# Optimization experiments

Measured on AMD Instinct MI355X. Metric: run time of the kernel, lower is better.

## Reference

```python
import jax, jax.numpy as jnp
import numpy as np

B, C, P = 16, 512, 4096


def setup_inputs() -> dict:
    key = jax.random.key(0)
    ks = jax.random.split(key, 7)
    s = 1.0 / np.sqrt(C)  # torch Conv1d default init scale
    return {
        "x": jax.random.normal(ks[0], (B, C, P), dtype=jnp.float32),
        "Wq": jax.random.uniform(ks[1], (C, C), jnp.float32, -s, s),
        "bq": jax.random.uniform(ks[2], (C,), jnp.float32, -s, s),
        "Wk": jax.random.uniform(ks[3], (C, C), jnp.float32, -s, s),
        "bk": jax.random.uniform(ks[4], (C,), jnp.float32, -s, s),
        "Wv": jax.random.uniform(ks[5], (C, C), jnp.float32, -s, s),
        "bv": jax.random.uniform(ks[6], (C,), jnp.float32, -s, s),
    }


def reference(x, Wq, bq, Wk, bk, Wv, bv):
    # 1x1 Conv1d == channel-mixing GEMM: out[b,o,p] = sum_i W[o,i] x[b,i,p] + b[o]
    q = jnp.einsum('oi,bip->bop', Wq, x) + bq[None, :, None]   # [B,C,P]
    k = jnp.einsum('oi,bip->bop', Wk, x) + bk[None, :, None]   # [B,C,P]
    v = jnp.einsum('oi,bip->bop', Wv, x) + bv[None, :, None]   # [B,C,P]
    energy = jnp.einsum('bcp,bdp->bcd', q, k)                  # [B,C,C] (unscaled)
    attn = jax.nn.softmax(energy, axis=-1)
    out = jnp.einsum('bcd,bdp->bcp', attn, v)                  # [B,C,P]
    return out
```

## Files before the change

kernel.cpp:

```cpp
#include <hip/hip_runtime.h>
#include <hip/hip_bf16.h>

#define CD 512
#define PD 4096
#define BD 16
#define GKS 8
#define NTRI 10

typedef __bf16 bf16x8 __attribute__((ext_vector_type(8)));
typedef float f32x4 __attribute__((ext_vector_type(4)));
typedef unsigned short u16x8 __attribute__((ext_vector_type(8)));
typedef unsigned short u16x4 __attribute__((ext_vector_type(4)));

__device__ __forceinline__ unsigned short f2bf(float f) {
  unsigned u = __builtin_bit_cast(unsigned, f);
  u += 0x7FFFu + ((u >> 16) & 1u);
  return (unsigned short)(u >> 16);
}
__device__ __forceinline__ float bf2f(unsigned short h) {
  unsigned u = ((unsigned)h) << 16;
  return __builtin_bit_cast(float, u);
}

__global__ void convert_w2(const float* __restrict__ Wq, const float* __restrict__ Wk,
                           unsigned short* __restrict__ Wqh, unsigned short* __restrict__ Wql,
                           unsigned short* __restrict__ Wkh, unsigned short* __restrict__ Wkl) {
  int i = blockIdx.x * 256 + threadIdx.x;
  if (i >= CD * CD) return;
  float q = Wq[i]; unsigned short qh = f2bf(q);
  Wqh[i] = qh; Wql[i] = f2bf(q - bf2f(qh));
  float k = Wk[i]; unsigned short kh = f2bf(k);
  Wkh[i] = kh; Wkl[i] = f2bf(k - bf2f(kh));
}

__global__ void transpose_wv(const float* __restrict__ Wv, unsigned short* __restrict__ Wvt) {
  __shared__ float tile[64][65];
  int o0 = blockIdx.x * 64, j0 = blockIdx.y * 64;
  int t = threadIdx.x, r = t >> 2, g = t & 3;
  const float* src = Wv + (size_t)(o0 + r) * CD + j0 + g * 16;
#pragma unroll
  for (int i = 0; i < 16; ++i) tile[r][g * 16 + i] = src[i];
  __syncthreads();
  u16x8 th[2];
#pragma unroll
  for (int i = 0; i < 16; ++i) th[i >> 3][i & 7] = f2bf(tile[g * 16 + i][r]);
  unsigned short* dst = Wvt + (size_t)(j0 + r) * CD + o0 + g * 16;
  *reinterpret_cast<u16x8*>(dst) = th[0];
  *reinterpret_cast<u16x8*>(dst + 8) = th[1];
}

__global__ void convert_x_stream(const float* __restrict__ x, unsigned short* __restrict__ xsh,
                                 unsigned short* __restrict__ xsl, float* __restrict__ r_part) {
  int z = blockIdx.y, c = blockIdx.x;
  int t = threadIdx.x;
  size_t rowo = ((size_t)z * CD + c) * PD;
  const float* src = x + rowo + t * 16;
  f32x4 v4[4];
  float s = 0.f;
#pragma unroll
  for (int j = 0; j < 4; ++j) {
    v4[j] = *reinterpret_cast<const f32x4*>(src + j * 4);
    s += v4[j][0] + v4[j][1] + v4[j][2] + v4[j][3];
  }
  u16x8 h[2], l[2];
#pragma unroll
  for (int j = 0; j < 4; ++j)
#pragma unroll
    for (int i = 0; i < 4; ++i) {
      int e = j * 4 + i;
      float f = v4[j][i];
      unsigned short hh = f2bf(f);
      h[e >> 3][e & 7] = hh;
      l[e >> 3][e & 7] = f2bf(f - bf2f(hh));
    }
  unsigned short* ph = xsh + rowo + t * 16;
  unsigned short* pl = xsl + rowo + t * 16;
  *reinterpret_cast<u16x8*>(ph) = h[0];
  *reinterpret_cast<u16x8*>(ph + 8) = h[1];
  *reinterpret_cast<u16x8*>(pl) = l[0];
  *reinterpret_cast<u16x8*>(pl + 8) = l[1];
  s += __shfl_xor(s, 1);
  s += __shfl_xor(s, 2);
  if ((t & 3) == 0) r_part[((size_t)z * CD + c) * 64 + (t >> 2)] = s;
}

__global__ void transpose_xh(const unsigned short* __restrict__ xsh,
                             unsigned short* __restrict__ xth) {
  __shared__ unsigned short sh[64][72];
  int z = blockIdx.z;
  int p0 = blockIdx.x * 64, c0 = blockIdx.y * 64;
  int t = threadIdx.x, r = t >> 2, g = t & 3;
  const unsigned short* src = xsh + ((size_t)z * CD + c0 + r) * PD + p0 + g * 16;
  *reinterpret_cast<u16x8*>(&sh[r][g * 16]) = *reinterpret_cast<const u16x8*>(src);
  *reinterpret_cast<u16x8*>(&sh[r][g * 16 + 8]) = *reinterpret_cast<const u16x8*>(src + 8);
  __syncthreads();
  u16x8 th[2];
#pragma unroll
  for (int i = 0; i < 16; ++i) th[i >> 3][i & 7] = sh[g * 16 + i][r];
  unsigned short* dst = xth + ((size_t)z * PD + p0 + r) * CD + c0 + g * 16;
  *reinterpret_cast<u16x8*>(dst) = th[0];
  *reinterpret_cast<u16x8*>(dst + 8) = th[1];
}

__global__ void uvw_kernel(const float* __restrict__ r_part, const float* __restrict__ Wq,
                           const float* __restrict__ bq, const float* __restrict__ Wk,
                           float* __restrict__ uw) {
  __shared__ float rl[CD];
  int z = blockIdx.x, rg = blockIdx.y;
  int t = threadIdx.x;
  for (int c = t; c < CD; c += 256) {
    const float* rp = r_part + ((size_t)z * CD + c) * 64;
    f32x4 s4 = *reinterpret_cast<const f32x4*>(rp);
#pragma unroll
    for (int pb = 4; pb < 64; pb += 4) s4 += *reinterpret_cast<const f32x4*>(rp + pb);
    rl[c] = s4[0] + s4[1] + s4[2] + s4[3];
  }
  __syncthreads();
  int lane = t & 63, w = t >> 6;
#pragma unroll
  for (int rr = 0; rr < 16; ++rr) {
    int c = rg * 64 + w * 16 + rr;
    const float* wq = Wq + (size_t)c * CD;
    const float* wk = Wk + (size_t)c * CD;
    float du = 0.f, dw = 0.f;
#pragma unroll
    for (int j = 0; j < 8; ++j) {
      float rv = rl[lane + 64 * j];
      du += wq[lane + 64 * j] * rv;
      dw += wk[lane + 64 * j] * rv;
    }
#pragma unroll
    for (int o = 32; o > 0; o >>= 1) {
      du += __shfl_xor(du, o);
      dw += __shfl_xor(dw, o);
    }
    if (lane == 0) {
      uw[(size_t)z * 2 * CD + c] = du + (float)PD * bq[c];
      uw[(size_t)z * 2 * CD + CD + c] = dw;
    }
  }
}

enum { EPI_F32 = 0, EPI_HILO = 1, EPI_BF16 = 2, EPI_ROWB = 3 };

template <int BM, int BN, int WM, int WN, int MODE, int EPI, bool TRI, int SPLITK = 1>
__global__ __launch_bounds__((BM / WM) * (BN / WN) * 64) void gemm2(
    const unsigned short* __restrict__ Ahi, const unsigned short* __restrict__ Alo,
    const unsigned short* __restrict__ Bhi, const unsigned short* __restrict__ Blo,
    long long sA, long long sB, int ldA, int ldB, int K,
    float* __restrict__ Cf, unsigned short* __restrict__ Chi, unsigned short* __restrict__ Clo,
    long long sC, int ldC, const float* __restrict__ bias, int gx, int gy) {
  constexpr int BK = 64;
  constexpr int WAVES = (BM / WM) * (BN / WN);
  constexpr int NSL = (MODE == 1) ? 2 : 1;
  constexpr int NPASS = (MODE == 2) ? 3 : 1;
  constexpr int MI = WM / 16, NI = WN / 16;
  constexpr int NWN = BN / WN;
  constexpr int CA = BM / 8, CB = BN / 8;
  constexpr int TOT = NSL * (CA + CB);
  constexpr bool COMPACT = TRI && (SPLITK > 1);
  __shared__ unsigned short lds[NSL * (BM + BN) * BK];

  int nwg = gridDim.x;
  int b = blockIdx.x;
  int q = nwg >> 3, r = nwg & 7, xcd = b & 7, pos = b >> 3;
  int wg = (xcd < r ? xcd * (q + 1) : r * (q + 1) + (xcd - r) * q) + pos;
  int bx, by, z, zc, tpi = 0, kbase = 0;
  if constexpr (TRI) {
    int tri = gy * (gy + 1) / 2;
    int perz = tri * SPLITK;
    z = wg / perz;
    int rem = wg - z * perz;
    int ks = rem / tri;
    tpi = rem - ks * tri;
    int tp = tpi;
    bx = 0;
    while (tp >= gy - bx) { tp -= gy - bx; ++bx; }
    by = bx + tp;
    kbase = ks * K;
    zc = z * SPLITK + ks;
  } else {
    by = wg % gy;
    int t2 = wg / gy;
    bx = t2 % gx;
    z = t2 / gx;
    zc = z;
  }

  const unsigned short* pA0 = Ahi + (size_t)z * sA + (size_t)bx * BM * ldA;
  const unsigned short* pB0 = Bhi + (size_t)z * sB + (size_t)by * BN * ldB;
  const unsigned short* pA1 = (MODE != 0) ? Alo + (size_t)z * sA + (size_t)bx * BM * ldA : pA0;
  const unsigned short* pB1 = (MODE != 0) ? Blo + (size_t)z * sB + (size_t)by * BN * ldB : pB0;

  int tid = threadIdx.x;
  int lane = tid & 63, wid = tid >> 6;
  int wr = wid / NWN, wc = wid % NWN;
  int lr = lane & 15, kh2 = lane >> 4;

  f32x4 acc[MI][NI] = {};

  for (int pass = 0; pass < NPASS; ++pass) {
    const unsigned short* cA = (MODE == 2 && pass == 2) ? pA1 : pA0;
    const unsigned short* cB = (MODE == 2 && pass == 1) ? pB1 : pB0;

    for (int k0 = kbase; k0 < kbase + K; k0 += BK) {
#pragma unroll
      for (int i = 0; i < TOT / WAVES; ++i) {
        int c = wid + i * WAVES;
        const unsigned short* srcb; int ldX, lofs, rb2;
        if constexpr (MODE == 1) {
          if (c < CA)            { srcb = pA0; ldX = ldA; lofs = c * 512;                  rb2 = c * 8; }
          else if (c < 2 * CA)   { srcb = pA1; ldX = ldA; lofs = BM * BK + (c - CA) * 512; rb2 = (c - CA) * 8; }
          else if (c < 2 * CA + CB) { int cc = c - 2 * CA; srcb = pB0; ldX = ldB;
                                      lofs = 2 * BM * BK + cc * 512;                       rb2 = cc * 8; }
          else                   { int cc = c - 2 * CA - CB; srcb = pB1; ldX = ldB;
                                   lofs = 2 * BM * BK + BN * BK + cc * 512;                rb2 = cc * 8; }
        } else {
          if (c < CA)            { srcb = cA; ldX = ldA; lofs = c * 512;                   rb2 = c * 8; }
          else                   { int cc = c - CA; srcb = cB; ldX = ldB;
                                   lofs = BM * BK + cc * 512;                              rb2 = cc * 8; }
        }
        int row = rb2 + (lane >> 3);
        const unsigned short* src =
            srcb + (size_t)row * ldX + k0 + (((lane & 7) ^ (row & 7)) << 3);
        __builtin_amdgcn_global_load_lds(
            (const __attribute__((address_space(1))) void*)src,
            (__attribute__((address_space(3))) void*)(lds + lofs), 16, 0, 0);
      }
      __syncthreads();

#pragma unroll
      for (int kk = 0; kk < BK / 32; ++kk) {
        bf16x8 ah[MI], al[MI], bh[NI], bl[NI];
#pragma unroll
        for (int m = 0; m < MI; ++m) {
          int row = wr * WM + m * 16 + lr;
          int so = ((((kk << 2) | kh2) ^ (row & 7)) << 3);
          ah[m] = *reinterpret_cast<const bf16x8*>(&lds[row * BK + so]);
          if constexpr (MODE == 1)
            al[m] = *reinterpret_cast<const bf16x8*>(&lds[BM * BK + row * BK + so]);
        }
#pragma unroll
        for (int n = 0; n < NI; ++n) {
          int row = wc * WN + n * 16 + lr;
          int so = ((((kk << 2) | kh2) ^ (row & 7)) << 3);
          bh[n] = *reinterpret_cast<const bf16x8*>(&lds[NSL * BM * BK + row * BK + so]);
          if constexpr (MODE == 1)
            bl[n] = *reinterpret_cast<const bf16x8*>(&lds[NSL * BM * BK + BN * BK + row * BK + so]);
        }
#pragma unroll
        for (int m = 0; m < MI; ++m)
#pragma unroll
          for (int n = 0; n < NI; ++n) {
            acc[m][n] = __builtin_amdgcn_mfma_f32_16x16x32_bf16(ah[m], bh[n], acc[m][n], 0, 0, 0);
            if constexpr (MODE == 1) {
              acc[m][n] = __builtin_amdgcn_mfma_f32_16x16x32_bf16(ah[m], bl[n], acc[m][n], 0, 0, 0);
              acc[m][n] = __builtin_amdgcn_mfma_f32_16x16x32_bf16(al[m], bh[n], acc[m][n], 0, 0, 0);
            }
          }
      }
      __syncthreads();
    }
  }

  int lg = lane >> 4;
#pragma unroll
  for (int m = 0; m < MI; ++m)
#pragma unroll
    for (int n = 0; n < NI; ++n) {
      int lcol = wc * WN + n * 16 + lr;
#pragma unroll
      for (int r4 = 0; r4 < 4; ++r4) {
        int lrow = wr * WM + m * 16 + lg * 4 + r4;
        float v = acc[m][n][r4];
        if constexpr (COMPACT) {
          size_t idx = (size_t)zc * sC + (size_t)tpi * (BM * BN) + (size_t)lrow * BN + lcol;
          Cf[idx] = v;
        } else {
          size_t idx = (size_t)zc * sC + (size_t)(bx * BM + lrow) * ldC + (by * BN + lcol);
          if constexpr (EPI == EPI_F32) {
            Cf[idx] = v;
          } else if constexpr (EPI == EPI_ROWB) {
            Cf[idx] = v + bias[(size_t)zc * CD + bx * BM + lrow];
          } else if constexpr (EPI == EPI_HILO) {
            unsigned short h = f2bf(v);
            Chi[idx] = h;
            Clo[idx] = f2bf(v - bf2f(h));
          } else {
            Chi[idx] = f2bf(v);
          }
        }
      }
    }
}

template <int KS>
__global__ void gram_reduce(const float* __restrict__ Gp,
                            unsigned short* __restrict__ Ghi, unsigned short* __restrict__ Glo) {
  int z = blockIdx.y;
  int tp = blockIdx.x;
  int b2 = tp, bx = 0;
  while (b2 >= 4 - bx) { b2 -= 4 - bx; ++bx; }
  int by = bx + b2;
  int t = threadIdx.x;
  const float* base = Gp + ((size_t)z * KS * NTRI + tp) * (128 * 128);
  size_t gb = (size_t)z * CD * CD;
#pragma unroll
  for (int it = 0; it < 16; ++it) {
    int lrow = it * 8 + (t >> 5);
    int lc = (t & 31) * 4;
    f32x4 s = *reinterpret_cast<const f32x4*>(base + (size_t)lrow * 128 + lc);
#pragma unroll
    for (int ks = 1; ks < KS; ++ks)
      s += *reinterpret_cast<const f32x4*>(base + (size_t)ks * NTRI * 128 * 128 +
                                           (size_t)lrow * 128 + lc);
    u16x4 h, l;
#pragma unroll
    for (int i = 0; i < 4; ++i) {
      unsigned short hh = f2bf(s[i]);
      h[i] = hh; l[i] = f2bf(s[i] - bf2f(hh));
    }
    size_t o = gb + (size_t)(bx * 128 + lrow) * CD + by * 128 + lc;
    *reinterpret_cast<u16x4*>(Ghi + o) = h;
    *reinterpret_cast<u16x4*>(Glo + o) = l;
  }
}

__global__ void mirror_g(unsigned short* __restrict__ Ghi, unsigned short* __restrict__ Glo) {
  __shared__ unsigned short shh[64][72], shl[64][72];
  int z = blockIdx.y;
  int pidx = blockIdx.x >> 2, sub = blockIdx.x & 3;
  int bx = 0, tp = pidx;
  while (tp >= 3 - bx) { tp -= 3 - bx; ++bx; }
  int by = bx + 1 + tp;
  int ti = bx * 2 + (sub & 1), tj = by * 2 + (sub >> 1);
  int t = threadIdx.x;
  int rr = t >> 2, cg = (t & 3) * 16;
  size_t gbase = (size_t)z * CD * CD;
  size_t so = gbase + (size_t)(ti * 64 + rr) * CD + tj * 64 + cg;
  *reinterpret_cast<u16x8*>(&shh[rr][cg]) = *reinterpret_cast<const u16x8*>(Ghi + so);
  *reinterpret_cast<u16x8*>(&shh[rr][cg + 8]) = *reinterpret_cast<const u16x8*>(Ghi + so + 8);
  *reinterpret_cast<u16x8*>(&shl[rr][cg]) = *reinterpret_cast<const u16x8*>(Glo + so);
  *reinterpret_cast<u16x8*>(&shl[rr][cg + 8]) = *reinterpret_cast<const u16x8*>(Glo + so + 8);
  __syncthreads();
  u16x8 oh, ol;
  size_t dst = gbase + (size_t)(tj * 64 + rr) * CD + ti * 64 + cg;
#pragma unroll
  for (int half = 0; half < 2; ++half) {
#pragma unroll
    for (int i = 0; i < 8; ++i) {
      oh[i] = shh[cg + half * 8 + i][rr];
      ol[i] = shl[cg + half * 8 + i][rr];
    }
    *reinterpret_cast<u16x8*>(Ghi + dst + half * 8) = oh;
    *reinterpret_cast<u16x8*>(Glo + dst + half * 8) = ol;
  }
}

__global__ void softmax_rows(const float* __restrict__ E, unsigned short* __restrict__ attn,
                             const float* __restrict__ bq, const float* __restrict__ bk,
                             const float* __restrict__ uw, const float* __restrict__ bv,
                             float* __restrict__ sv) {
  int lane = threadIdx.x & 63, wid = threadIdx.x >> 6;
  size_t row = (size_t)blockIdx.x * 4 + wid;
  int z = (int)(row >> 9), c = (int)(row & 511);
  float uc = uw[(size_t)z * 2 * CD + c];
  float bqc = bq[c];
  const float* wp = uw + (size_t)z * 2 * CD + CD;
  const float* e = E + row * CD;
  int d0 = lane * 8;
  const float4* ep = reinterpret_cast<const float4*>(e + d0);
  float4 a = ep[0], b4 = ep[1];
  float4 k0 = *reinterpret_cast<const float4*>(bk + d0);
  float4 k1 = *reinterpret_cast<const float4*>(bk + d0 + 4);
  float4 w0 = *reinterpret_cast<const float4*>(wp + d0);
  float4 w1 = *reinterpret_cast<const float4*>(wp + d0 + 4);
  float v[8] = {a.x + uc * k0.x + bqc * w0.x, a.y + uc * k0.y + bqc * w0.y,
                a.z + uc * k0.z + bqc * w0.z, a.w + uc * k0.w + bqc * w0.w,
                b4.x + uc * k1.x + bqc * w1.x, b4.y + uc * k1.y + bqc * w1.y,
                b4.z + uc * k1.z + bqc * w1.z, b4.w + uc * k1.w + bqc * w1.w};
  float m = v[0];
#pragma unroll
  for (int i = 1; i < 8; ++i) m = fmaxf(m, v[i]);
  for (int o = 32; o > 0; o >>= 1) m = fmaxf(m, __shfl_xor(m, o));
  float s = 0.f;
#pragma unroll
  for (int i = 0; i < 8; ++i) { v[i] = __expf(v[i] - m); s += v[i]; }
  for (int o = 32; o > 0; o >>= 1) s += __shfl_xor(s, o);
  float rinv = 1.0f / s;
  float4 bv0 = *reinterpret_cast<const float4*>(bv + d0);
  float4 bv1 = *reinterpret_cast<const float4*>(bv + d0 + 4);
  u16x4 h0, h1;
  float svp = 0.f;
#pragma unroll
  for (int i = 0; i < 4; ++i) {
    h0[i] = f2bf(v[i] * rinv);
    h1[i] = f2bf(v[4 + i] * rinv);
    svp += bf2f(h0[i]) * (&bv0.x)[i] + bf2f(h1[i]) * (&bv1.x)[i];
  }
  for (int o = 32; o > 0; o >>= 1) svp += __shfl_xor(svp, o);
  if (lane == 0) sv[row] = svp;
  unsigned short* op = attn + row * CD + d0;
  *reinterpret_cast<u16x4*>(op) = h0;
  *reinterpret_cast<u16x4*>(op + 4) = h1;
}

extern "C" void kernel_launch(void* const* d_in, const int* in_sizes, int n_in,
                              void* d_out, int out_size, void* d_ws, size_t ws_size,
                              hipStream_t stream) {
  (void)in_sizes; (void)n_in; (void)out_size;
  const float* x  = (const float*)d_in[0];
  const float* Wq = (const float*)d_in[1];
  const float* bq = (const float*)d_in[2];
  const float* Wk = (const float*)d_in[3];
  const float* bk = (const float*)d_in[4];
  const float* Wv = (const float*)d_in[5];
  const float* bv = (const float*)d_in[6];
  float* out = (float*)d_out;

  char* base = (char*)d_ws;
  size_t off = 0;
  auto carve = [&](size_t bytes) -> char* {
    char* p = base + off;
    off += (bytes + 255) & ~(size_t)255;
    return p;
  };
  const size_t WB = (size_t)CD * CD * 2;
  unsigned short* Wqh = (unsigned short*)carve(WB);
  unsigned short* Wql = (unsigned short*)carve(WB);
  unsigned short* Wkh = (unsigned short*)carve(WB);
  unsigned short* Wkl = (unsigned short*)carve(WB);
  unsigned short* Wvt = (unsigned short*)carve(WB);

  const size_t CP = (size_t)CD * PD;
  const size_t GG = (size_t)CD * CD;
  const size_t EE = (size_t)CD * CD;
  const size_t PERZC = (size_t)NTRI * 128 * 128;
  const size_t GPB = (size_t)GKS * PERZC;
  const size_t per_batch = 3 * CP * 2 + 4 * GG * 2 + (size_t)CD * 64 * 4 + 2 * CD * 4 +
                           (size_t)CD * 4 + EE * 4 + EE * 2 + GPB * 4 + 8192;
  size_t rem = (ws_size > off + 4096) ? (ws_size - off - 4096) : 0;
  int nb = (int)(rem / per_batch);
  if (nb < 1) nb = 1;
  if (nb > BD) nb = BD;

  unsigned short* xsh = (unsigned short*)carve((size_t)nb * CP * 2);
  unsigned short* xsl = (unsigned short*)carve((size_t)nb * CP * 2);
  unsigned short* xth = (unsigned short*)carve((size_t)nb * CP * 2);
  unsigned short* Ghi = (unsigned short*)carve((size_t)nb * GG * 2);
  unsigned short* Glo = (unsigned short*)carve((size_t)nb * GG * 2);
  unsigned short* Thi = (unsigned short*)carve((size_t)nb * GG * 2);
  unsigned short* Tlo = (unsigned short*)carve((size_t)nb * GG * 2);
  float*          r_part = (float*)carve((size_t)nb * CD * 64 * 4);
  float*          uw  = (float*)carve((size_t)nb * 2 * CD * 4);
  float*          sv  = (float*)carve((size_t)nb * CD * 4);
  float*          E   = (float*)carve((size_t)nb * EE * 4);
  unsigned short* att = (unsigned short*)carve((size_t)nb * EE * 2);
  float*          Gpart = (float*)carve((size_t)nb * GPB * 4);

  convert_w2<<<dim3((CD * CD + 255) / 256), 256, 0, stream>>>(Wq, Wk, Wqh, Wql, Wkh, Wkl);
  transpose_wv<<<dim3(8, 8), 256, 0, stream>>>(Wv, Wvt);

  for (int b0 = 0; b0 < BD; b0 += nb) {
    int cb = (BD - b0 < nb) ? (BD - b0) : nb;

    convert_x_stream<<<dim3(CD, cb), 256, 0, stream>>>(
        x + (size_t)b0 * CP, xsh, xsl, r_part);

    transpose_xh<<<dim3(PD / 64, CD / 64, cb), 256, 0, stream>>>(xsh, xth);

    uvw_kernel<<<dim3(cb, 8), 256, 0, stream>>>(r_part, Wq, bq, Wk, uw);

    gemm2<128, 128, 64, 32, 2, EPI_F32, true, GKS><<<NTRI * GKS * cb, 512, 0, stream>>>(
        xsh, xsl, xsh, xsl, (long long)CP, (long long)CP, PD, PD, PD / GKS,
        Gpart, nullptr, nullptr, (long long)PERZC, 128, nullptr, 4, 4);

    gram_reduce<GKS><<<dim3(NTRI, cb), 256, 0, stream>>>(Gpart, Ghi, Glo);

    mirror_g<<<dim3(24, cb), 256, 0, stream>>>(Ghi, Glo);

    gemm2<64, 64, 32, 32, 1, EPI_HILO, false><<<8 * 8 * cb, 256, 0, stream>>>(
        Wqh, Wql, Ghi, Glo, 0, (long long)GG, CD, CD, CD,
        nullptr, Thi, Tlo, (long long)GG, CD, nullptr, 8, 8);

    gemm2<64, 64, 32, 32, 1, EPI_F32, false><<<8 * 8 * cb, 256, 0, stream>>>(
        Thi, Tlo, Wkh, Wkl, (long long)GG, 0, CD, CD, CD,
        E, nullptr, nullptr, (long long)EE, CD, nullptr, 8, 8);

    softmax_rows<<<dim3(cb * CD / 4), 256, 0, stream>>>(E, att, bq, bk, uw, bv, sv);

    gemm2<64, 64, 32, 32, 0, EPI_BF16, false><<<8 * 8 * cb, 256, 0, stream>>>(
        att, nullptr, Wvt, nullptr, (long long)EE, 0, CD, CD, CD,
        nullptr, Thi, nullptr, (long long)GG, CD, nullptr, 8, 8);

    gemm2<128, 128, 64, 64, 0, EPI_ROWB, false><<<4 * 32 * cb, 256, 0, stream>>>(
        Thi, nullptr, xth, nullptr, (long long)GG, (long long)CP, CD, CD, CD,
        out + (size_t)b0 * CP, nullptr, nullptr, (long long)CP, PD, sv, 4, 32);
  }
}
```

Baseline: 341.7 us.

## Switch Gram GEMM to fused hi/lo mode and fold mirroring into reduce

The Gram-matrix GEMM drops its three sequential passes over K (hi*hi, hi*lo, lo*hi) and uses MODE 1 instead, which loads hi and lo tiles together and issues three MFMAs per k-step. This cuts loop overhead and the two extra rounds of global loads and barriers, but doubles LDS use per block and raises register pressure. Separately, the mirror_g kernel is removed, and gram_reduce now writes each transposed off-diagonal tile itself through shared memory. That saves a launch and a full re-read of G, at the cost of extra barriers inside the reduce.

```diff
diff --git a/kernel.cpp b/kernel.cpp
--- a/kernel.cpp
+++ b/kernel.cpp
@@ -153,7 +153,6 @@
   constexpr int BK = 64;
   constexpr int WAVES = (BM / WM) * (BN / WN);
   constexpr int NSL = (MODE == 1) ? 2 : 1;
-  constexpr int NPASS = (MODE == 2) ? 3 : 1;
   constexpr int MI = WM / 16, NI = WN / 16;
   constexpr int NWN = BN / WN;
   constexpr int CA = BM / 8, CB = BN / 8;
@@ -199,68 +198,63 @@
 
   f32x4 acc[MI][NI] = {};
 
-  for (int pass = 0; pass < NPASS; ++pass) {
-    const unsigned short* cA = (MODE == 2 && pass == 2) ? pA1 : pA0;
-    const unsigned short* cB = (MODE == 2 && pass == 1) ? pB1 : pB0;
-
-    for (int k0 = kbase; k0 < kbase + K; k0 += BK) {
-#pragma unroll
-      for (int i = 0; i < TOT / WAVES; ++i) {
-        int c = wid + i * WAVES;
-        const unsigned short* srcb; int ldX, lofs, rb2;
-        if constexpr (MODE == 1) {
-          if (c < CA)            { srcb = pA0; ldX = ldA; lofs = c * 512;                  rb2 = c * 8; }
-          else if (c < 2 * CA)   { srcb = pA1; ldX = ldA; lofs = BM * BK + (c - CA) * 512; rb2 = (c - CA) * 8; }
-          else if (c < 2 * CA + CB) { int cc = c - 2 * CA; srcb = pB0; ldX = ldB;
-                                      lofs = 2 * BM * BK + cc * 512;                       rb2 = cc * 8; }
-          else                   { int cc = c - 2 * CA - CB; srcb = pB1; ldX = ldB;
-                                   lofs = 2 * BM * BK + BN * BK + cc * 512;                rb2 = cc * 8; }
-        } else {
-          if (c < CA)            { srcb = cA; ldX = ldA; lofs = c * 512;                   rb2 = c * 8; }
-          else                   { int cc = c - CA; srcb = cB; ldX = ldB;
-                                   lofs = BM * BK + cc * 512;                              rb2 = cc * 8; }
+  for (int k0 = kbase; k0 < kbase + K; k0 += BK) {
+#pragma unroll
+    for (int i = 0; i < TOT / WAVES; ++i) {
+      int c = wid + i * WAVES;
+      const unsigned short* srcb; int ldX, lofs, rb2;
+      if constexpr (MODE == 1) {
+        if (c < CA)            { srcb = pA0; ldX = ldA; lofs = c * 512;                  rb2 = c * 8; }
+        else if (c < 2 * CA)   { srcb = pA1; ldX = ldA; lofs = BM * BK + (c - CA) * 512; rb2 = (c - CA) * 8; }
+        else if (c < 2 * CA + CB) { int cc = c - 2 * CA; srcb = pB0; ldX = ldB;
+                                    lofs = 2 * BM * BK + cc * 512;                       rb2 = cc * 8; }
+        else                   { int cc = c - 2 * CA - CB; srcb = pB1; ldX = ldB;
+                                 lofs = 2 * BM * BK + BN * BK + cc * 512;                rb2 = cc * 8; }
+      } else {
+        if (c < CA)            { srcb = pA0; ldX = ldA; lofs = c * 512;                  rb2 = c * 8; }
+        else                   { int cc = c - CA; srcb = pB0; ldX = ldB;
+                                 lofs = BM * BK + cc * 512;                              rb2 = cc * 8; }
+      }
+      int row = rb2 + (lane >> 3);
+      const unsigned short* src =
+          srcb + (size_t)row * ldX + k0 + (((lane & 7) ^ (row & 7)) << 3);
+      __builtin_amdgcn_global_load_lds(
+          (const __attribute__((address_space(1))) void*)src,
+          (__attribute__((address_space(3))) void*)(lds + lofs), 16, 0, 0);
+    }
+    __syncthreads();
+
+#pragma unroll
+    for (int kk = 0; kk < BK / 32; ++kk) {
+      bf16x8 ah[MI], al[MI], bh[NI], bl[NI];
+#pragma unroll
+      for (int m = 0; m < MI; ++m) {
+        int row = wr * WM + m * 16 + lr;
+        int so = ((((kk << 2) | kh2) ^ (row & 7)) << 3);
+        ah[m] = *reinterpret_cast<const bf16x8*>(&lds[row * BK + so]);
+        if constexpr (MODE == 1)
+          al[m] = *reinterpret_cast<const bf16x8*>(&lds[BM * BK + row * BK + so]);
+      }
+#pragma unroll
+      for (int n = 0; n < NI; ++n) {
+        int row = wc * WN + n * 16 + lr;
+        int so = ((((kk << 2) | kh2) ^ (row & 7)) << 3);
+        bh[n] = *reinterpret_cast<const bf16x8*>(&lds[NSL * BM * BK + row * BK + so]);
+        if constexpr (MODE == 1)
+          bl[n] = *reinterpret_cast<const bf16x8*>(&lds[NSL * BM * BK + BN * BK + row * BK + so]);
+      }
+#pragma unroll
+      for (int m = 0; m < MI; ++m)
+#pragma unroll
+        for (int n = 0; n < NI; ++n) {
+          acc[m][n] = __builtin_amdgcn_mfma_f32_16x16x32_bf16(ah[m], bh[n], acc[m][n], 0, 0, 0);
+          if constexpr (MODE == 1) {
+            acc[m][n] = __builtin_amdgcn_mfma_f32_16x16x32_bf16(ah[m], bl[n], acc[m][n], 0, 0, 0);
+            acc[m][n] = __builtin_amdgcn_mfma_f32_16x16x32_bf16(al[m], bh[n], acc[m][n], 0, 0, 0);
+          }
         }
-        int row = rb2 + (lane >> 3);
-        const unsigned short* src =
-            srcb + (size_t)row * ldX + k0 + (((lane & 7) ^ (row & 7)) << 3);
-        __builtin_amdgcn_global_load_lds(
-            (const __attribute__((address_space(1))) void*)src,
-            (__attribute__((address_space(3))) void*)(lds + lofs), 16, 0, 0);
-      }
-      __syncthreads();
-
-#pragma unroll
-      for (int kk = 0; kk < BK / 32; ++kk) {
-        bf16x8 ah[MI], al[MI], bh[NI], bl[NI];
-#pragma unroll
-        for (int m = 0; m < MI; ++m) {
-          int row = wr * WM + m * 16 + lr;
-          int so = ((((kk << 2) | kh2) ^ (row & 7)) << 3);
-          ah[m] = *reinterpret_cast<const bf16x8*>(&lds[row * BK + so]);
-          if constexpr (MODE == 1)
-            al[m] = *reinterpret_cast<const bf16x8*>(&lds[BM * BK + row * BK + so]);
-        }
-#pragma unroll
-        for (int n = 0; n < NI; ++n) {
-          int row = wc * WN + n * 16 + lr;
-          int so = ((((kk << 2) | kh2) ^ (row & 7)) << 3);
-          bh[n] = *reinterpret_cast<const bf16x8*>(&lds[NSL * BM * BK + row * BK + so]);
-          if constexpr (MODE == 1)
-            bl[n] = *reinterpret_cast<const bf16x8*>(&lds[NSL * BM * BK + BN * BK + row * BK + so]);
-        }
-#pragma unroll
-        for (int m = 0; m < MI; ++m)
-#pragma unroll
-          for (int n = 0; n < NI; ++n) {
-            acc[m][n] = __builtin_amdgcn_mfma_f32_16x16x32_bf16(ah[m], bh[n], acc[m][n], 0, 0, 0);
-            if constexpr (MODE == 1) {
-              acc[m][n] = __builtin_amdgcn_mfma_f32_16x16x32_bf16(ah[m], bl[n], acc[m][n], 0, 0, 0);
-              acc[m][n] = __builtin_amdgcn_mfma_f32_16x16x32_bf16(al[m], bh[n], acc[m][n], 0, 0, 0);
-            }
-          }
-      }
-      __syncthreads();
-    }
+    }
+    __syncthreads();
   }
 
   int lg = lane >> 4;
@@ -297,64 +291,63 @@
 template <int KS>
 __global__ void gram_reduce(const float* __restrict__ Gp,
                             unsigned short* __restrict__ Ghi, unsigned short* __restrict__ Glo) {
+  __shared__ unsigned short shh[64][72], shl[64][72];
   int z = blockIdx.y;
   int tp = blockIdx.x;
   int b2 = tp, bx = 0;
   while (b2 >= 4 - bx) { b2 -= 4 - bx; ++bx; }
   int by = bx + b2;
   int t = threadIdx.x;
+  int rr = t >> 2, cg = (t & 3) * 16;
   const float* base = Gp + ((size_t)z * KS * NTRI + tp) * (128 * 128);
   size_t gb = (size_t)z * CD * CD;
-#pragma unroll
-  for (int it = 0; it < 16; ++it) {
-    int lrow = it * 8 + (t >> 5);
-    int lc = (t & 31) * 4;
-    f32x4 s = *reinterpret_cast<const f32x4*>(base + (size_t)lrow * 128 + lc);
-#pragma unroll
-    for (int ks = 1; ks < KS; ++ks)
-      s += *reinterpret_cast<const f32x4*>(base + (size_t)ks * NTRI * 128 * 128 +
-                                           (size_t)lrow * 128 + lc);
-    u16x4 h, l;
-#pragma unroll
-    for (int i = 0; i < 4; ++i) {
-      unsigned short hh = f2bf(s[i]);
-      h[i] = hh; l[i] = f2bf(s[i] - bf2f(hh));
-    }
-    size_t o = gb + (size_t)(bx * 128 + lrow) * CD + by * 128 + lc;
-    *reinterpret_cast<u16x4*>(Ghi + o) = h;
-    *reinterpret_cast<u16x4*>(Glo + o) = l;
-  }
-}
-
-__global__ void mirror_g(unsigned short* __restrict__ Ghi, unsigned short* __restrict__ Glo) {
-  __shared__ unsigned short shh[64][72], shl[64][72];
-  int z = blockIdx.y;
-  int pidx = blockIdx.x >> 2, sub = blockIdx.x & 3;
-  int bx = 0, tp = pidx;
-  while (tp >= 3 - bx) { tp -= 3 - bx; ++bx; }
-  int by = bx + 1 + tp;
-  int ti = bx * 2 + (sub & 1), tj = by * 2 + (sub >> 1);
-  int t = threadIdx.x;
-  int rr = t >> 2, cg = (t & 3) * 16;
-  size_t gbase = (size_t)z * CD * CD;
-  size_t so = gbase + (size_t)(ti * 64 + rr) * CD + tj * 64 + cg;
-  *reinterpret_cast<u16x8*>(&shh[rr][cg]) = *reinterpret_cast<const u16x8*>(Ghi + so);
-  *reinterpret_cast<u16x8*>(&shh[rr][cg + 8]) = *reinterpret_cast<const u16x8*>(Ghi + so + 8);
-  *reinterpret_cast<u16x8*>(&shl[rr][cg]) = *reinterpret_cast<const u16x8*>(Glo + so);
-  *reinterpret_cast<u16x8*>(&shl[rr][cg + 8]) = *reinterpret_cast<const u16x8*>(Glo + so + 8);
-  __syncthreads();
-  u16x8 oh, ol;
-  size_t dst = gbase + (size_t)(tj * 64 + rr) * CD + ti * 64 + cg;
-#pragma unroll
-  for (int half = 0; half < 2; ++half) {
-#pragma unroll
-    for (int i = 0; i < 8; ++i) {
-      oh[i] = shh[cg + half * 8 + i][rr];
-      ol[i] = shl[cg + half * 8 + i][rr];
-    }
-    *reinterpret_cast<u16x8*>(Ghi + dst + half * 8) = oh;
-    *reinterpret_cast<u16x8*>(Glo + dst + half * 8) = ol;
-  }
+  bool offd = (bx != by);
+#pragma unroll
+  for (int si = 0; si < 2; ++si)
+#pragma unroll
+    for (int sj = 0; sj < 2; ++sj) {
+      const float* p0 = base + (size_t)(si * 64 + rr) * 128 + sj * 64 + cg;
+      f32x4 s[4];
+#pragma unroll
+      for (int q4 = 0; q4 < 4; ++q4) s[q4] = *reinterpret_cast<const f32x4*>(p0 + q4 * 4);
+      for (int ks = 1; ks < KS; ++ks) {
+        const float* pk = p0 + (size_t)ks * NTRI * 128 * 128;
+#pragma unroll
+        for (int q4 = 0; q4 < 4; ++q4) s[q4] += *reinterpret_cast<const f32x4*>(pk + q4 * 4);
+      }
+      u16x8 h[2], l[2];
+#pragma unroll
+      for (int e = 0; e < 16; ++e) {
+        float v = s[e >> 2][e & 3];
+        unsigned short hh = f2bf(v);
+        h[e >> 3][e & 7] = hh;
+        l[e >> 3][e & 7] = f2bf(v - bf2f(hh));
+      }
+      size_t o = gb + (size_t)(bx * 128 + si * 64 + rr) * CD + by * 128 + sj * 64 + cg;
+      *reinterpret_cast<u16x8*>(Ghi + o) = h[0];
+      *reinterpret_cast<u16x8*>(Ghi + o + 8) = h[1];
+      *reinterpret_cast<u16x8*>(Glo + o) = l[0];
+      *reinterpret_cast<u16x8*>(Glo + o + 8) = l[1];
+      if (offd) {
+        *reinterpret_cast<u16x8*>(&shh[rr][cg]) = h[0];
+        *reinterpret_cast<u16x8*>(&shh[rr][cg + 8]) = h[1];
+        *reinterpret_cast<u16x8*>(&shl[rr][cg]) = l[0];
+        *reinterpret_cast<u16x8*>(&shl[rr][cg + 8]) = l[1];
+        __syncthreads();
+        u16x8 oh[2], ol[2];
+#pragma unroll
+        for (int i = 0; i < 16; ++i) {
+          oh[i >> 3][i & 7] = shh[cg + i][rr];
+          ol[i >> 3][i & 7] = shl[cg + i][rr];
+        }
+        size_t d = gb + (size_t)(by * 128 + sj * 64 + rr) * CD + bx * 128 + si * 64 + cg;
+        *reinterpret_cast<u16x8*>(Ghi + d) = oh[0];
+        *reinterpret_cast<u16x8*>(Ghi + d + 8) = oh[1];
+        *reinterpret_cast<u16x8*>(Glo + d) = ol[0];
+        *reinterpret_cast<u16x8*>(Glo + d + 8) = ol[1];
+        __syncthreads();
+      }
+    }
 }
 
 __global__ void softmax_rows(const float* __restrict__ E, unsigned short* __restrict__ attn,
@@ -471,13 +464,11 @@
 
     uvw_kernel<<<dim3(cb, 8), 256, 0, stream>>>(r_part, Wq, bq, Wk, uw);
 
-    gemm2<128, 128, 64, 32, 2, EPI_F32, true, GKS><<<NTRI * GKS * cb, 512, 0, stream>>>(
+    gemm2<128, 128, 64, 32, 1, EPI_F32, true, GKS><<<NTRI * GKS * cb, 512, 0, stream>>>(
         xsh, xsl, xsh, xsl, (long long)CP, (long long)CP, PD, PD, PD / GKS,
         Gpart, nullptr, nullptr, (long long)PERZC, 128, nullptr, 4, 4);
 
     gram_reduce<GKS><<<dim3(NTRI, cb), 256, 0, stream>>>(Gpart, Ghi, Glo);
-
-    mirror_g<<<dim3(24, cb), 256, 0, stream>>>(Ghi, Glo);
 
     gemm2<64, 64, 32, 32, 1, EPI_HILO, false><<<8 * 8 * cb, 256, 0, stream>>>(
         Wqh, Wql, Ghi, Glo, 0, (long long)GG, CD, CD, CD,
```

New measurement: 336.2 us. No clear change (-1.6%).
